# Optimization experiments

Hardware: AMD Instinct MI355X
Metric: run time of the kernel (lower is better)

Reference implementation:

```python
import jax, jax.numpy as jnp
import numpy as np

NUM_HEADS = 16


def _apply_rotary(x, cos, sin):
    # x: [B, H, L, D]; cos/sin: [L, D//2] broadcast over B, H
    d = x.shape[-1] // 2
    x1, x2 = x[..., :d], x[..., d:]
    return jnp.concatenate([x1 * cos - x2 * sin, x2 * cos + x1 * sin], axis=-1)


def setup_inputs() -> dict:
    key = jax.random.key(0)
    k_x, k_c, k_s, k_qkv, k_w, k_b = jax.random.split(key, 6)
    B, L, dim = 2, 2048, 2048
    head_dim = dim // NUM_HEADS
    x = jax.random.normal(k_x, (B, L, dim), dtype=jnp.float32)
    cos = jax.random.uniform(k_c, (L, head_dim // 2), dtype=jnp.float32)
    sin = jax.random.uniform(k_s, (L, head_dim // 2), dtype=jnp.float32)
    scale = 1.0 / np.sqrt(dim)
    w_qkv = jax.random.normal(k_qkv, (dim, 3 * dim), dtype=jnp.float32) * scale
    w_out = jax.random.normal(k_w, (dim, dim), dtype=jnp.float32) * scale
    b_out = jax.random.normal(k_b, (dim,), dtype=jnp.float32) * 0.01
    return {"x": x, "cos": cos, "sin": sin, "w_qkv": w_qkv, "w_out": w_out, "b_out": b_out}


def reference(x, cos, sin, w_qkv, w_out, b_out):
    B, L, dim = x.shape
    H = NUM_HEADS
    D = dim // H
    # fused QKV projection (no bias), split to q,k,v: [B, H, L, D]
    qkv = (x @ w_qkv).reshape(B, L, 3, H, D)
    qkv = jnp.transpose(qkv, (2, 0, 3, 1, 4))
    q, k, v = qkv[0], qkv[1], qkv[2]
    q = _apply_rotary(q, cos, sin)
    k = _apply_rotary(k, cos, sin)
    # scaled dot-product attention (non-causal, scale = 1/sqrt(D))
    scores = jnp.einsum('bhqd,bhkd->bhqk', q, k) / jnp.sqrt(jnp.asarray(D, q.dtype))
    attn = jax.nn.softmax(scores, axis=-1)
    out = jnp.einsum('bhqk,bhkd->bhqd', attn, v)  # [B, H, L, D]
    out = jnp.transpose(out, (0, 2, 1, 3)).reshape(B, L, dim)
    return out @ w_out + b_out
```

## Files before the change

### kernel.cpp

```cpp
#include <hip/hip_runtime.h>
#include <cstdint>
#include <cstddef>

typedef unsigned short u16;
typedef __attribute__((ext_vector_type(2))) unsigned short u16x2;
typedef __attribute__((ext_vector_type(4))) unsigned short u16x4;
typedef __attribute__((ext_vector_type(8))) unsigned short u16x8;
typedef __attribute__((ext_vector_type(4))) float f32x4;
typedef __attribute__((ext_vector_type(8))) __bf16 bf16x8;

#define B_    2
#define L_    2048
#define DIM_  2048
#define H_    16
#define HD_   128
#define NQKV_ 6144
#define M_    4096

__device__ __forceinline__ float b2f(u16 h) {
  union { unsigned u; float f; } v; v.u = ((unsigned)h) << 16; return v.f;
}
__device__ __forceinline__ u16 f2bf(float f) {
  unsigned u = __float_as_uint(f);
  u += 0x7fffu + ((u >> 16) & 1u);
  return (u16)(u >> 16);
}
__device__ __forceinline__ f32x4 mfma16(bf16x8 a, bf16x8 b, f32x4 c) {
  return __builtin_amdgcn_mfma_f32_16x16x32_bf16(a, b, c, 0, 0, 0);
}
__device__ __forceinline__ void async16(const void* g, void* l) {
  __builtin_amdgcn_global_load_lds(
      (const __attribute__((address_space(1))) unsigned*)g,
      (__attribute__((address_space(3))) unsigned*)l, 16, 0, 0);
}

__device__ __forceinline__ void transpose_tile(
    const float* __restrict__ src, u16* __restrict__ dst,
    u16 (*tile)[66], int tid, int r0, int c0, int R, int C) {
  #pragma unroll
  for (int i = 0; i < 4; ++i) {
    int f = i * 256 + tid;
    int r = f >> 4, c4 = (f & 15) * 4;
    f32x4 v = *(const f32x4*)&src[(size_t)(r0 + r) * C + (c0 + c4)];
    #pragma unroll
    for (int j = 0; j < 4; ++j) tile[r][c4 + j] = f2bf(v[j]);
  }
  __syncthreads();
  #pragma unroll
  for (int i = 0; i < 4; ++i) {
    int f = i * 256 + tid;
    int cr = f >> 4, rp = (f & 15) * 4;
    u16x4 o = {tile[rp][cr], tile[rp + 1][cr], tile[rp + 2][cr], tile[rp + 3][cr]};
    *(u16x4*)&dst[(size_t)(c0 + cr) * R + (r0 + rp)] = o;
  }
}

__global__ __launch_bounds__(256) void prepass_k(
    const float* __restrict__ x, u16* __restrict__ xbf,
    const float* __restrict__ wqkv, u16* __restrict__ wqkvT) {
  __shared__ u16 tile[64][66];
  const int bid = blockIdx.x;
  if (bid < 4096) {
    int i = (bid * 256 + threadIdx.x) * 8;
    f32x4 a = *(const f32x4*)&x[i];
    f32x4 b = *(const f32x4*)&x[i + 4];
    u16x8 o;
    #pragma unroll
    for (int j = 0; j < 4; ++j) { o[j] = f2bf(a[j]); o[j + 4] = f2bf(b[j]); }
    *(u16x8*)&xbf[i] = o;
  } else {
    const int t = bid - 4096;
    const int by = t / 96, bx = t - by * 96;
    transpose_tile(wqkv, wqkvT, tile, threadIdx.x, by * 64, bx * 64, 2048, 6144);
  }
}

__global__ __launch_bounds__(256) void post_k(
    const float* __restrict__ wout, u16* __restrict__ woutT,
    u16* __restrict__ Q, u16* __restrict__ Kb,
    const float* __restrict__ cs, const float* __restrict__ sn) {
  __shared__ u16 tile[64][66];
  const int bid = blockIdx.x;
  if (bid < 1024) {
    const int bx = bid & 31, by = bid >> 5;
    transpose_tile(wout, woutT, tile, threadIdx.x, by * 64, bx * 64, 2048, 2048);
  } else {
    const int rb = bid - 1024;
    const int tid = threadIdx.x;
    const int tensor = tid >> 7;
    const int rsub = (tid >> 4) & 7;
    const int j = tid & 15;
    const int row = rb * 8 + rsub;
    const int l = row & (L_ - 1);
    u16* P = tensor ? Kb : Q;
    size_t base = (size_t)row * HD_ + j * 8;
    u16x8 v = *(const u16x8*)&P[base];
    f32x4 c = *(const f32x4*)&cs[l * 64 + j * 4];
    f32x4 s = *(const f32x4*)&sn[l * 64 + j * 4];
    u16x8 o;
    #pragma unroll
    for (int e = 0; e < 4; ++e) {
      float x1 = b2f(v[2 * e]), x2 = b2f(v[2 * e + 1]);
      o[2 * e]     = f2bf(x1 * c[e] - x2 * s[e]);
      o[2 * e + 1] = f2bf(x2 * c[e] + x1 * s[e]);
    }
    *(u16x8*)&P[base] = o;
  }
}

template <int MODE>
__global__ __launch_bounds__(256) void gemm_bt(
    const u16* __restrict__ A, const u16* __restrict__ Bt,
    u16* __restrict__ D0, u16* __restrict__ D1, u16* __restrict__ D2,
    const float* __restrict__ bias, float* __restrict__ outp,
    int M, int N, int K) {
  __shared__ __align__(16) u16 Alds[128 * 64];
  __shared__ __align__(16) u16 Blds[128 * 64];
  const int tid = threadIdx.x;
  const int wave = tid >> 6;
  const int wm = wave >> 1, wn = wave & 1;
  const int ln = tid & 15, qd = (tid >> 4) & 3;
  const int m0 = blockIdx.y * 128, n0 = blockIdx.x * 128;

  f32x4 acc[4][4];
  #pragma unroll
  for (int i = 0; i < 4; ++i)
    #pragma unroll
    for (int j = 0; j < 4; ++j) acc[i][j] = (f32x4){0.f, 0.f, 0.f, 0.f};

  for (int k0 = 0; k0 < K; k0 += 64) {
    __syncthreads();
    #pragma unroll
    for (int j = 0; j < 4; ++j) {
      int oe = j * 2048 + tid * 8;
      int se = oe ^ (((oe >> 6) & 7) << 3);
      int r = oe >> 6, c = se & 63;
      async16(&A[(size_t)(m0 + r) * K + (k0 + c)], &Alds[j * 2048 + wave * 512]);
      async16(&Bt[(size_t)(n0 + r) * K + (k0 + c)], &Blds[j * 2048 + wave * 512]);
    }
    __syncthreads();
    #pragma unroll
    for (int kk = 0; kk < 2; ++kk) {
      bf16x8 af[4], bfr[4];
      #pragma unroll
      for (int mi = 0; mi < 4; ++mi) {
        int arow = wm * 64 + mi * 16 + ln;
        af[mi] = *(const bf16x8*)&Alds[arow * 64 +
                     ((kk * 32 + qd * 8) ^ ((arow & 7) << 3))];
      }
      #pragma unroll
      for (int ni = 0; ni < 4; ++ni) {
        int brow = wn * 64 + ni * 16 + ln;
        bfr[ni] = *(const bf16x8*)&Blds[brow * 64 +
                     ((kk * 32 + qd * 8) ^ ((brow & 7) << 3))];
      }
      #pragma unroll
      for (int mi = 0; mi < 4; ++mi)
        #pragma unroll
        for (int ni = 0; ni < 4; ++ni)
          acc[mi][ni] = mfma16(af[mi], bfr[ni], acc[mi][ni]);
    }
  }

  if (MODE == 2) {
    #pragma unroll
    for (int mi = 0; mi < 4; ++mi)
      #pragma unroll
      for (int ni = 0; ni < 4; ++ni)
        #pragma unroll
        for (int r = 0; r < 4; ++r) {
          int row = m0 + wm * 64 + mi * 16 + qd * 4 + r;
          int col = n0 + wn * 64 + ni * 16 + ln;
          outp[(size_t)row * N + col] = acc[mi][ni][r] + bias[col];
        }
  } else {
    const int t  = n0 >> 11;
    const int hh = (n0 & 2047) >> 7;
    const int bb = m0 >> 11;
    const int l0 = (m0 & 2047) + wm * 64;
    const int d0    = (t != 2) ? (((ln) << 1) | wn) : (wn * 64 + ln);
    const int dstep = (t != 2) ? 32 : 16;
    u16* dst = (t == 0) ? D0 : ((t == 1) ? D1 : D2);
    u16* basep = dst + ((size_t)(bb * H_ + hh) * L_) * HD_;
    #pragma unroll
    for (int mi = 0; mi < 4; ++mi)
      #pragma unroll
      for (int r = 0; r < 4; ++r) {
        int l = l0 + mi * 16 + qd * 4 + r;
        #pragma unroll
        for (int ni = 0; ni < 4; ++ni)
          basep[(size_t)l * HD_ + d0 + ni * dstep] = f2bf(acc[mi][ni][r]);
      }
  }
}

__global__ __launch_bounds__(256, 4) void attn_k(
    const u16* __restrict__ Q, const u16* __restrict__ Kb,
    const u16* __restrict__ V, u16* __restrict__ Ao) {
  __shared__ __align__(16) u16 lds[25600];
  u16* Klds = lds;
  u16* Vlds = lds + 8192;
  u16* Plds = lds + 16384;
  const int tid = threadIdx.x;
  const int w = tid >> 6, lane = tid & 63;
  const int ln = lane & 15, qd = lane >> 4;
  const int qt = blockIdx.x, bh = blockIdx.y;
  const int b = bh >> 4, h = bh & 15;
  const size_t slab = (size_t)bh * (L_ * HD_);
  const int vd0 = 2 * lane;

  #pragma unroll
  for (int j = 0; j < 8; ++j) {
    int oe = j * 2048 + w * 512 + lane * 8;
    int se = oe ^ (((oe >> 7) & 7) << 3);
    async16(&Q[slab + (size_t)qt * 16384 + se], &lds[j * 2048 + w * 512]);
  }
  __syncthreads();
  bf16x8 aq[2][4];
  #pragma unroll
  for (int mi = 0; mi < 2; ++mi) {
    int qrow = w * 32 + mi * 16 + ln;
    #pragma unroll
    for (int kc = 0; kc < 4; ++kc)
      aq[mi][kc] = *(const bf16x8*)&lds[qrow * 128 +
                                        ((kc * 32 + qd * 8) ^ ((qrow & 7) << 3))];
  }

  f32x4 o[2][8];
  #pragma unroll
  for (int i = 0; i < 2; ++i)
    #pragma unroll
    for (int j = 0; j < 8; ++j) o[i][j] = (f32x4){0.f, 0.f, 0.f, 0.f};
  float mst[2][4], lsum[2][4];
  #pragma unroll
  for (int i = 0; i < 2; ++i)
    #pragma unroll
    for (int r = 0; r < 4; ++r) { mst[i][r] = -1e30f; lsum[i][r] = 0.f; }
  const float SC = 0.12751744f;

  for (int it = 0; it < 32; ++it) {
    unsigned vv[2][8];
    #pragma unroll
    for (int n2 = 0; n2 < 2; ++n2) {
      int key0 = (w + n2 * 4) * 8;
      #pragma unroll
      for (int e = 0; e < 8; ++e)
        vv[n2][e] = *(const unsigned*)&V[slab + (size_t)(it * 64 + key0 + e) * 128 + vd0];
    }
    __syncthreads();
    #pragma unroll
    for (int j = 0; j < 4; ++j) {
      int oe = j * 2048 + w * 512 + lane * 8;
      int se = oe ^ (((oe >> 7) & 7) << 3);
      async16(&Kb[slab + (size_t)it * 8192 + se], &Klds[j * 2048 + w * 512]);
    }
    {
      int swz = (lane & 7) << 3;
      #pragma unroll
      for (int n2 = 0; n2 < 2; ++n2) {
        int key0 = (w + n2 * 4) * 8;
        u16x8 lo, hi;
        #pragma unroll
        for (int e = 0; e < 8; ++e) {
          lo[e] = (u16)(vv[n2][e] & 0xffffu);
          hi[e] = (u16)(vv[n2][e] >> 16);
        }
        *(u16x8*)&Vlds[vd0 * 64 + (key0 ^ swz)] = lo;
        *(u16x8*)&Vlds[(vd0 + 1) * 64 + (key0 ^ swz)] = hi;
      }
    }
    __syncthreads();

    f32x4 sa[2][4];
    #pragma unroll
    for (int i = 0; i < 2; ++i)
      #pragma unroll
      for (int j = 0; j < 4; ++j) sa[i][j] = (f32x4){0.f, 0.f, 0.f, 0.f};
    #pragma unroll
    for (int kc = 0; kc < 4; ++kc) {
      bf16x8 bk[4];
      #pragma unroll
      for (int ni = 0; ni < 4; ++ni) {
        int krow = ni * 16 + ln;
        bk[ni] = *(const bf16x8*)&Klds[krow * 128 +
                                       ((kc * 32 + qd * 8) ^ ((krow & 7) << 3))];
      }
      #pragma unroll
      for (int mi = 0; mi < 2; ++mi)
        #pragma unroll
        for (int ni = 0; ni < 4; ++ni)
          sa[mi][ni] = mfma16(aq[mi][kc], bk[ni], sa[mi][ni]);
    }

    #pragma unroll
    for (int mi = 0; mi < 2; ++mi) {
      #pragma unroll
      for (int r = 0; r < 4; ++r) {
        float tmax = -1e30f;
        #pragma unroll
        for (int ni = 0; ni < 4; ++ni) tmax = fmaxf(tmax, sa[mi][ni][r]);
        tmax *= SC;
        tmax = fmaxf(tmax, __shfl_xor(tmax, 1));
        tmax = fmaxf(tmax, __shfl_xor(tmax, 2));
        tmax = fmaxf(tmax, __shfl_xor(tmax, 4));
        tmax = fmaxf(tmax, __shfl_xor(tmax, 8));
        float mnew = fmaxf(mst[mi][r], tmax);
        float alpha = exp2f(mst[mi][r] - mnew);
        float p[4], rs = 0.f;
        #pragma unroll
        for (int ni = 0; ni < 4; ++ni) {
          p[ni] = exp2f(sa[mi][ni][r] * SC - mnew);
          rs += p[ni];
        }
        lsum[mi][r] = lsum[mi][r] * alpha + rs;
        mst[mi][r] = mnew;
        #pragma unroll
        for (int di = 0; di < 8; ++di) o[mi][di][r] *= alpha;
        #pragma unroll
        for (int ni = 0; ni < 4; ++ni)
          Plds[(w * 32 + mi * 16 + qd * 4 + r) * 72 + ni * 16 + ln] = f2bf(p[ni]);
      }
    }


    #pragma unroll
    for (int kc = 0; kc < 2; ++kc) {
      bf16x8 ap[2];
      #pragma unroll
      for (int mi = 0; mi < 2; ++mi)
        ap[mi] = *(const bf16x8*)&Plds[(w * 32 + mi * 16 + ln) * 72 + kc * 32 + qd * 8];
      #pragma unroll
      for (int di = 0; di < 8; ++di) {
        int vrow = di * 16 + ln;
        bf16x8 bv = *(const bf16x8*)&Vlds[vrow * 64 +
                         ((kc * 32 + qd * 8) ^ (((vrow >> 1) & 7) << 3))];
        o[0][di] = mfma16(ap[0], bv, o[0][di]);
        o[1][di] = mfma16(ap[1], bv, o[1][di]);
      }
    }
  }

  #pragma unroll
  for (int mi = 0; mi < 2; ++mi) {
    #pragma unroll
    for (int r = 0; r < 4; ++r) {
      float l = lsum[mi][r];
      l += __shfl_xor(l, 1);
      l += __shfl_xor(l, 2);
      l += __shfl_xor(l, 4);
      l += __shfl_xor(l, 8);
      float inv = 1.0f / l;
      int lrow = qt * 128 + w * 32 + mi * 16 + qd * 4 + r;
      size_t orow = ((size_t)b * L_ + lrow) * DIM_ + (size_t)h * HD_;
      #pragma unroll
      for (int di = 0; di < 8; ++di)
        Ao[orow + di * 16 + ln] = f2bf(o[mi][di][r] * inv);
    }
  }
}

extern "C" void kernel_launch(void* const* d_in, const int* in_sizes, int n_in,
                              void* d_out, int out_size, void* d_ws, size_t ws_size,
                              hipStream_t stream) {
  const float* x    = (const float*)d_in[0];
  const float* cs   = (const float*)d_in[1];
  const float* sn   = (const float*)d_in[2];
  const float* wqkv = (const float*)d_in[3];
  const float* wout = (const float*)d_in[4];
  const float* bias = (const float*)d_in[5];
  u16* ws = (u16*)d_ws;

  u16* wqkvT = ws;
  u16* woutT = ws;
  u16* xbfAo = wqkvT + 12582912;
  u16* Qb    = xbfAo + 8388608;
  u16* Kbuf  = Qb + 8388608;
  u16* Vbuf  = Kbuf + 8388608;

  prepass_k<<<dim3(7168), 256, 0, stream>>>(x, xbfAo, wqkv, wqkvT);
  gemm_bt<1><<<dim3(48, 32), 256, 0, stream>>>(
      xbfAo, wqkvT, Qb, Kbuf, Vbuf, nullptr, nullptr, M_, NQKV_, DIM_);
  post_k<<<dim3(9216), 256, 0, stream>>>(wout, woutT, Qb, Kbuf, cs, sn);
  attn_k<<<dim3(16, 32), 256, 0, stream>>>(Qb, Kbuf, Vbuf, xbfAo);
  gemm_bt<2><<<dim3(16, 32), 256, 0, stream>>>(
      xbfAo, woutT, nullptr, nullptr, nullptr, bias, (float*)d_out, M_, DIM_, DIM_);
}
```

Before: 452.1 us.

## Double attention query tile to 256 rows with 512-thread blocks sharing K/V tiles

The attention kernel now runs 8 waves per block, each owning 32 query rows, so a block covers 256 queries and the grid halves. Each K/V tile staged in LDS is shared by twice as many queries, which halves global K/V traffic and spreads the staging work across more threads. The P buffer switches from a padded stride of 72 to a stride of 64 with an XOR swizzle, keeping bank-conflict avoidance while fitting the larger tile. The risks are fewer blocks (256) to spread across the CUs and higher LDS use per block, which may limit occupancy.

New measurement: 897.7 us. 1.99x slower.

```diff
diff --git a/kernel.cpp b/kernel.cpp
--- a/kernel.cpp
+++ b/kernel.cpp
@@ -194,10 +194,10 @@
   }
 }
 
-__global__ __launch_bounds__(256, 4) void attn_k(
+__global__ __launch_bounds__(512, 4) void attn_k(
     const u16* __restrict__ Q, const u16* __restrict__ Kb,
     const u16* __restrict__ V, u16* __restrict__ Ao) {
-  __shared__ __align__(16) u16 lds[25600];
+  __shared__ __align__(16) u16 lds[32768];
   u16* Klds = lds;
   u16* Vlds = lds + 8192;
   u16* Plds = lds + 16384;
@@ -211,9 +211,9 @@
 
   #pragma unroll
   for (int j = 0; j < 8; ++j) {
-    int oe = j * 2048 + w * 512 + lane * 8;
+    int oe = j * 4096 + tid * 8;
     int se = oe ^ (((oe >> 7) & 7) << 3);
-    async16(&Q[slab + (size_t)qt * 16384 + se], &lds[j * 2048 + w * 512]);
+    async16(&Q[slab + (size_t)qt * 32768 + se], &lds[j * 4096 + w * 512 + lane * 8]);
   }
   __syncthreads();
   bf16x8 aq[2][4];
@@ -239,35 +239,31 @@
   const float SC = 0.12751744f;
 
   for (int it = 0; it < 32; ++it) {
-    unsigned vv[2][8];
-    #pragma unroll
-    for (int n2 = 0; n2 < 2; ++n2) {
-      int key0 = (w + n2 * 4) * 8;
+    unsigned vv[8];
+    {
+      int key0 = w * 8;
       #pragma unroll
       for (int e = 0; e < 8; ++e)
-        vv[n2][e] = *(const unsigned*)&V[slab + (size_t)(it * 64 + key0 + e) * 128 + vd0];
+        vv[e] = *(const unsigned*)&V[slab + (size_t)(it * 64 + key0 + e) * 128 + vd0];
     }
     __syncthreads();
     #pragma unroll
-    for (int j = 0; j < 4; ++j) {
-      int oe = j * 2048 + w * 512 + lane * 8;
+    for (int j = 0; j < 2; ++j) {
+      int oe = j * 4096 + tid * 8;
       int se = oe ^ (((oe >> 7) & 7) << 3);
-      async16(&Kb[slab + (size_t)it * 8192 + se], &Klds[j * 2048 + w * 512]);
+      async16(&Kb[slab + (size_t)it * 8192 + se], &Klds[j * 4096 + w * 512 + lane * 8]);
     }
     {
+      int key0 = w * 8;
       int swz = (lane & 7) << 3;
-      #pragma unroll
-      for (int n2 = 0; n2 < 2; ++n2) {
-        int key0 = (w + n2 * 4) * 8;
-        u16x8 lo, hi;
-        #pragma unroll
-        for (int e = 0; e < 8; ++e) {
-          lo[e] = (u16)(vv[n2][e] & 0xffffu);
-          hi[e] = (u16)(vv[n2][e] >> 16);
-        }
-        *(u16x8*)&Vlds[vd0 * 64 + (key0 ^ swz)] = lo;
-        *(u16x8*)&Vlds[(vd0 + 1) * 64 + (key0 ^ swz)] = hi;
-      }
+      u16x8 lo, hi;
+      #pragma unroll
+      for (int e = 0; e < 8; ++e) {
+        lo[e] = (u16)(vv[e] & 0xffffu);
+        hi[e] = (u16)(vv[e] >> 16);
+      }
+      *(u16x8*)&Vlds[vd0 * 64 + (key0 ^ swz)] = lo;
+      *(u16x8*)&Vlds[(vd0 + 1) * 64 + (key0 ^ swz)] = hi;
     }
     __syncthreads();
 
@@ -316,9 +312,10 @@
         mst[mi][r] = mnew;
         #pragma unroll
         for (int di = 0; di < 8; ++di) o[mi][di][r] *= alpha;
+        int prow = w * 32 + mi * 16 + qd * 4 + r;
         #pragma unroll
         for (int ni = 0; ni < 4; ++ni)
-          Plds[(w * 32 + mi * 16 + qd * 4 + r) * 72 + ni * 16 + ln] = f2bf(p[ni]);
+          Plds[prow * 64 + ((ni * 16 + ln) ^ ((prow & 7) << 3))] = f2bf(p[ni]);
       }
     }
 
@@ -327,8 +324,11 @@
     for (int kc = 0; kc < 2; ++kc) {
       bf16x8 ap[2];
       #pragma unroll
-      for (int mi = 0; mi < 2; ++mi)
-        ap[mi] = *(const bf16x8*)&Plds[(w * 32 + mi * 16 + ln) * 72 + kc * 32 + qd * 8];
+      for (int mi = 0; mi < 2; ++mi) {
+        int prow = w * 32 + mi * 16 + ln;
+        ap[mi] = *(const bf16x8*)&Plds[prow * 64 +
+                                       ((kc * 32 + qd * 8) ^ ((prow & 7) << 3))];
+      }
       #pragma unroll
       for (int di = 0; di < 8; ++di) {
         int vrow = di * 16 + ln;
@@ -350,7 +350,7 @@
       l += __shfl_xor(l, 4);
       l += __shfl_xor(l, 8);
       float inv = 1.0f / l;
-      int lrow = qt * 128 + w * 32 + mi * 16 + qd * 4 + r;
+      int lrow = qt * 256 + w * 32 + mi * 16 + qd * 4 + r;
       size_t orow = ((size_t)b * L_ + lrow) * DIM_ + (size_t)h * HD_;
       #pragma unroll
       for (int di = 0; di < 8; ++di)
@@ -381,7 +381,7 @@
   gemm_bt<1><<<dim3(48, 32), 256, 0, stream>>>(
       xbfAo, wqkvT, Qb, Kbuf, Vbuf, nullptr, nullptr, M_, NQKV_, DIM_);
   post_k<<<dim3(9216), 256, 0, stream>>>(wout, woutT, Qb, Kbuf, cs, sn);
-  attn_k<<<dim3(16, 32), 256, 0, stream>>>(Qb, Kbuf, Vbuf, xbfAo);
+  attn_k<<<dim3(8, 32), 512, 0, stream>>>(Qb, Kbuf, Vbuf, xbfAo);
   gemm_bt<2><<<dim3(16, 32), 256, 0, stream>>>(
       xbfAo, woutT, nullptr, nullptr, nullptr, bias, (float*)d_out, M_, DIM_, DIM_);
 }
```
